# Optimization experiments

Measured on AMD Instinct MI355X. Metric: run time of the kernel, lower is better.

## Reference

```python
import jax, jax.numpy as jnp
import numpy as np


def conv2d(x, w, b=None, pad=0):
    # x: [B,C,H,W], w: [O,I,kh,kw]
    out = jax.lax.conv_general_dilated(
        x, w, window_strides=(1, 1), padding=[(pad, pad), (pad, pad)],
        dimension_numbers=('NCHW', 'OIHW', 'NCHW'))
    if b is not None:
        out = out + b[None, :, None, None]
    return out


def setup_inputs() -> dict:
    key = jax.random.key(0)
    ks = jax.random.split(key, 10)
    B, C, W, H, N, G = 8, 256, 64, 64, 1024, 32
    s = jnp.float32(0.02)  # small init so softmax is not saturated
    return {
        'input_graph': jax.random.normal(ks[0], (B, N, G), jnp.float32),
        'input_image': jax.random.normal(ks[1], (B, C, W, H), jnp.float32),
        'Wq': jax.random.normal(ks[2], (C, C), jnp.float32) * s,
        'bq': jnp.zeros((C,), jnp.float32),
        'Wk': jax.random.normal(ks[3], (C, G), jnp.float32) * s,
        'bk': jnp.zeros((C,), jnp.float32),
        'Wv': jax.random.normal(ks[4], (C, G), jnp.float32) * s,
        'bv': jnp.zeros((C,), jnp.float32),
        'conv1_w': jax.random.normal(ks[5], (C, C, 1, 1), jnp.float32) * s,
        'bn_gamma': jnp.ones((C,), jnp.float32),
        'bn_beta': jnp.zeros((C,), jnp.float32),
        'bn_mean': jnp.zeros((C,), jnp.float32),
        'bn_var': jnp.ones((C,), jnp.float32),
        'conv2_w': jax.random.normal(ks[6], (C, C, 3, 3), jnp.float32) * s,
        'conv2_b': jnp.zeros((C,), jnp.float32),
        'conv3_w': jax.random.normal(ks[7], (C, C, 1, 1), jnp.float32) * s,
        'conv3_b': jnp.zeros((C,), jnp.float32),
    }


def reference(input_graph, input_image, Wq, bq, Wk, bk, Wv, bv,
              conv1_w, bn_gamma, bn_beta, bn_mean, bn_var,
              conv2_w, conv2_b, conv3_w, conv3_b):
    B, C, W, H = input_image.shape
    P = W * H
    g = jnp.transpose(input_graph, (0, 2, 1))  # [B,G,N]
    # 1x1 conv1d projections == per-position matmuls
    K = jnp.einsum('og,bgn->bon', Wk, g) + bk[None, :, None]   # [B,C,N]
    V = jnp.einsum('og,bgn->bon', Wv, g) + bv[None, :, None]   # [B,C,N]
    x = input_image.reshape(B, C, P)
    Q = jnp.einsum('oc,bcp->bop', Wq, x) + bq[None, :, None]   # [B,C,P]
    # att[b,p,n] = sum_c Q[b,c,p] * K[b,c,n]  (Q was permuted to [B,P,C] in torch)
    att = jnp.einsum('bcp,bcn->bpn', Q, K) / jnp.sqrt(jnp.float32(C))
    # NOTE: original applies Softmax(dim=1) -> over the P (pixel) axis
    att = jax.nn.softmax(att, axis=1)
    # message = V @ att^T : [B,C,N] x [B,N,P] -> [B,C,P]
    msg = jnp.einsum('bcn,bpn->bcp', V, att).reshape(B, C, W, H)
    # Conv_Bn_Activation: 1x1 conv (no bias) + BN (inference) + LeakyReLU(0.1)
    h = conv2d(msg, conv1_w)
    inv = jax.lax.rsqrt(bn_var + jnp.float32(1e-5))
    h = (h - bn_mean[None, :, None, None]) * (bn_gamma * inv)[None, :, None, None] + bn_beta[None, :, None, None]
    h = jnp.where(h > 0, h, jnp.float32(0.1) * h)
    h = conv2d(h, conv2_w, conv2_b, pad=1)  # 3x3, pad 1
    return input_image + conv2d(h, conv3_w, conv3_b)  # 1x1
```

## Files before the change

### kernel.cpp

```cpp
#include <hip/hip_runtime.h>
#include <hip/hip_bf16.h>

typedef __hip_bfloat16 bf16;
typedef unsigned short u16;
typedef __attribute__((ext_vector_type(8))) short  b8v;
typedef __attribute__((ext_vector_type(8))) unsigned short u16x8;
typedef __attribute__((ext_vector_type(4))) unsigned short u16x4;
typedef __attribute__((ext_vector_type(4))) float f32x4;

static __device__ __forceinline__ float us2f(u16 s) {
    unsigned int u = ((unsigned int)s) << 16;
    return __builtin_bit_cast(float, u);
}
static __device__ __forceinline__ u16 f2us(float x) {
    union { bf16 h; u16 s; } v; v.h = __float2bfloat16(x); return v.s;
}
static __device__ __forceinline__ float b2f(bf16 x) { return __bfloat162float(x); }
static __device__ __forceinline__ bf16 f2b(float x) { return __float2bfloat16(x); }
static __device__ __forceinline__ float toF(float x) { return x; }
static __device__ __forceinline__ float toF(bf16 x)  { return b2f(x); }
static __device__ __forceinline__ void stor(float* p, float v) { *p = v; }
static __device__ __forceinline__ void stor(bf16* p,  float v) { *p = f2b(v); }

static __device__ __forceinline__ void gload16(const u16* g, u16* l) {
    __builtin_amdgcn_global_load_lds(
        (const __attribute__((address_space(1))) unsigned int*)g,
        (__attribute__((address_space(3))) unsigned int*)l,
        16, 0, 0);
}


__global__ __launch_bounds__(256) void cast_f2b4(const float* __restrict__ src,
                                                 u16* __restrict__ dst, int n4)
{
    int i = blockIdx.x * 256 + threadIdx.x;
    if (i < n4) {
        float4 v = ((const float4*)src)[i];
        u16x4 o = { f2us(v.x), f2us(v.y), f2us(v.z), f2us(v.w) };
        ((u16x4*)dst)[i] = o;
    }
}

__global__ __launch_bounds__(256) void repack_w2(const float* __restrict__ src,
                                                 u16* __restrict__ dst)
{
    int idx = blockIdx.x * 256 + threadIdx.x;
    int o = idx / 2304, k = idx - o * 2304;
    int tap = k >> 8, c = k & 255;
    dst[idx] = f2us(src[(o * 256 + c) * 9 + tap]);
}

__global__ __launch_bounds__(256) void transpose_cast_x(const float* __restrict__ x,
                                                        u16* __restrict__ xT, int C, int P)
{
    __shared__ u16 t[64][72];
    const int b = blockIdx.z, c0 = blockIdx.y * 64, p0 = blockIdx.x * 64;
    const int tid = threadIdx.x;
    const int r = tid >> 2, q = tid & 3;
    const float* src = x + ((size_t)b * C + c0 + r) * P + p0 + q * 16;
#pragma unroll
    for (int i = 0; i < 16; i++) t[q * 16 + i][r] = f2us(src[i]);
    __syncthreads();
    u16* dst = xT + ((size_t)b * P + p0 + r) * C + c0 + q * 16;
    *(u16x8*)dst       = *(u16x8*)&t[r][q * 16];
    *(u16x8*)(dst + 8) = *(u16x8*)&t[r][q * 16 + 8];
}

template<int EPI, typename TA, typename TB, typename TC>
__global__ __launch_bounds__(256) void gemm_any(
    const TA* __restrict__ A, const TB* __restrict__ B, TC* __restrict__ C,
    int M, int Nn, int Kd,
    long saM, long saK, long aB,
    long sbK, long sbN, long bB,
    long scM, long scN, long cB,
    float scale, const float* __restrict__ bias)
{
    __shared__ float As[16][65];
    __shared__ float Bs[16][65];
    const int b  = blockIdx.z;
    const TA* Ab = A + (long)b * aB;
    const TB* Bb = B + (long)b * bB;
    const int m0 = blockIdx.y * 64, n0 = blockIdx.x * 64;
    const int tid = threadIdx.x;
    const int tx = tid & 15, ty = tid >> 4;
    const bool kfA = (saK == 1);
    const bool nfB = (sbN == 1);
    float acc[4][4] = {};

    for (int k0 = 0; k0 < Kd; k0 += 16) {
#pragma unroll
        for (int i = 0; i < 4; i++) {
            int idx = tid + i * 256; int mm, kk;
            if (kfA) { kk = idx & 15; mm = idx >> 4; }
            else     { mm = idx & 63; kk = idx >> 6; }
            As[kk][mm] = toF(Ab[(long)(m0 + mm) * saM + (long)(k0 + kk) * saK]);
        }
#pragma unroll
        for (int i = 0; i < 4; i++) {
            int idx = tid + i * 256; int nn, kk;
            if (nfB) { nn = idx & 63; kk = idx >> 6; }
            else     { kk = idx & 15; nn = idx >> 4; }
            Bs[kk][nn] = toF(Bb[(long)(k0 + kk) * sbK + (long)(n0 + nn) * sbN]);
        }
        __syncthreads();
#pragma unroll
        for (int kk = 0; kk < 16; kk++) {
            float a[4], bb[4];
#pragma unroll
            for (int i = 0; i < 4; i++) a[i]  = As[kk][ty * 4 + i];
#pragma unroll
            for (int j = 0; j < 4; j++) bb[j] = Bs[kk][tx * 4 + j];
#pragma unroll
            for (int i = 0; i < 4; i++)
#pragma unroll
                for (int j = 0; j < 4; j++) acc[i][j] += a[i] * bb[j];
        }
        __syncthreads();
    }
#pragma unroll
    for (int i = 0; i < 4; i++) {
        int m = m0 + ty * 4 + i;
        float add0 = (EPI == 0 && bias) ? bias[m] : 0.f;
#pragma unroll
        for (int j = 0; j < 4; j++) {
            int n = n0 + tx * 4 + j;
            float v = acc[i][j] * scale + add0;
            if (EPI == 3 && bias) v += bias[n];
            stor(&C[(long)b * cB + (long)m * scM + (long)n * scN], v);
        }
    }
}

template<int EPI, bool CT, typename TC, int NTILE>
__global__ __launch_bounds__(256) void gemm_mfma(
    const u16* __restrict__ A, const u16* __restrict__ Bt, TC* __restrict__ Cc,
    int M, int N, int K, int lda, int ldb, int ldc,
    long aBat, long bBat, long cBat,
    float scale, const float* __restrict__ bias,
    const float* __restrict__ gamma, const float* __restrict__ beta,
    const float* __restrict__ mean,  const float* __restrict__ var,
    const float* __restrict__ resid, long rBat, int ldr,
    float* __restrict__ csum)
{
    constexpr int NI = NTILE / 32;
    __shared__ u16 Al[128 * 32];
    __shared__ u16 Bl[NTILE * 32];
    __shared__ float red[(EPI == 3) ? 256 : 1];
    __shared__ u16 tbuf[(EPI == 3) ? 64 * 136 : 1];
    const int bat = blockIdx.z;
    const int m0 = blockIdx.y * 128, n0 = blockIdx.x * NTILE;
    const int tid = threadIdx.x;
    const int lane = tid & 63, wid = tid >> 6;
    const int wr = wid >> 1, wc = wid & 1;
    const int fr = lane & 15, fq = lane >> 4;
    const int sc = ((lane & 3) ^ ((lane >> 3) & 3)) * 8;
    const int axs = (fq ^ ((fr >> 1) & 3)) * 8;

    const u16* gA = A  + (size_t)bat * aBat + (size_t)(m0 + wid * 32 + (lane >> 2)) * lda + sc;
    const u16* gB = Bt + (size_t)bat * bBat + (size_t)(n0 + wid * (NTILE / 4) + (lane >> 2)) * ldb + sc;
    u16* lA = &Al[(wid * 32) * 32];
    u16* lB = &Bl[(wid * (NTILE / 4)) * 32];
    const size_t a16 = (size_t)16 * lda, b16 = (size_t)16 * ldb;

    f32x4 acc[4][NI];
#pragma unroll
    for (int i = 0; i < 4; i++)
#pragma unroll
        for (int j = 0; j < NI; j++) acc[i][j] = (f32x4){0.f, 0.f, 0.f, 0.f};

    for (int k0 = 0; k0 < K; k0 += 32) {
        gload16(gA + k0,       lA);
        gload16(gA + k0 + a16, lA + 16 * 32);
        gload16(gB + k0,       lB);
        if constexpr (NTILE == 128) gload16(gB + k0 + b16, lB + 16 * 32);
        __syncthreads();
        b8v a[4], b[NI];
#pragma unroll
        for (int mi = 0; mi < 4; mi++) a[mi] = *(const b8v*)&Al[(wr * 64 + mi * 16 + fr) * 32 + axs];
#pragma unroll
        for (int ni = 0; ni < NI; ni++) b[ni] = *(const b8v*)&Bl[(wc * (NTILE / 2) + ni * 16 + fr) * 32 + axs];
#pragma unroll
        for (int mi = 0; mi < 4; mi++)
#pragma unroll
            for (int ni = 0; ni < NI; ni++)
                acc[mi][ni] = __builtin_amdgcn_mfma_f32_16x16x32_bf16(a[mi], b[ni], acc[mi][ni], 0, 0, 0);
        __syncthreads();
    }

    const int mbase = m0 + wr * 64, nbase = n0 + wc * (NTILE / 2);

    if constexpr (EPI == 3) {
        float cs[NI];
#pragma unroll
        for (int ni = 0; ni < NI; ni++) cs[ni] = 0.f;
#pragma unroll
        for (int h = 0; h < 2; h++) {
#pragma unroll
            for (int mh = 0; mh < 2; mh++) {
                const int mi = h * 2 + mh;
                const int trow = wr * 32 + mh * 16 + fq * 4;
#pragma unroll
                for (int ni = 0; ni < NI; ni++) {
                    const int n = nbase + ni * 16 + fr;
                    const float tqv = bias ? bias[(size_t)bat * N + n] : 0.f;
                    f32x4 v = acc[mi][ni];
#pragma unroll
                    for (int j = 0; j < 4; j++) {
                        float x = __expf((v[j] + tqv) * scale);
                        cs[ni] += x;
                        tbuf[(trow + j) * 136 + wc * 64 + ni * 16 + fr] = f2us(x);
                    }
                }
            }
            __syncthreads();
#pragma unroll
            for (int it = 0; it < 4; it++) {
                const int idx = it * 256 + tid;
                const int row = idx >> 4, ng = idx & 15;
                const int m = m0 + (row >> 5) * 64 + h * 32 + (row & 31);
                u16x8 v8 = *(const u16x8*)&tbuf[row * 136 + ng * 8];
                *(u16x8*)((u16*)Cc + (size_t)bat * cBat + (size_t)m * ldc + n0 + ng * 8) = v8;
            }
            __syncthreads();
        }
#pragma unroll
        for (int ni = 0; ni < NI; ni++) {
            float s = cs[ni];
            s += __shfl_xor(s, 16, 64);
            s += __shfl_xor(s, 32, 64);
            if (fq == 0) red[wr * 128 + wc * 64 + ni * 16 + fr] = s;
        }
        __syncthreads();
        if (tid < NTILE) {
            float s = red[tid] + red[128 + tid];
            csum[((size_t)bat * gridDim.y + blockIdx.y) * ldc + n0 + tid] = s;
        }
        return;
    }

#pragma unroll
    for (int mi = 0; mi < 4; mi++) {
        float esc[4], ead[4];
#pragma unroll
        for (int j = 0; j < 4; j++) {
            int m = mbase + mi * 16 + fq * 4 + j;
            if (EPI == 1) {
                float sc2 = gamma[m] * rsqrtf(var[m] + 1e-5f);
                esc[j] = sc2; ead[j] = beta[m] - mean[m] * sc2;
            } else {
                esc[j] = scale;
                ead[j] = ((EPI == 0 || EPI == 2) && bias) ? bias[m] : 0.f;
            }
        }
#pragma unroll
        for (int ni = 0; ni < NI; ni++) {
            f32x4 v = acc[mi][ni];
            const int n = nbase + ni * 16 + fr;
            if (CT) {
                const int mb = mbase + mi * 16 + fq * 4;
                if constexpr (EPI == 4) {
                    const float bb = bias ? bias[n] : 0.f;
                    float4 rv = *(const float4*)&resid[(size_t)bat * rBat + (size_t)n * ldr + mb];
                    float4 o4;
                    o4.x = v[0] * scale + bb + rv.x;
                    o4.y = v[1] * scale + bb + rv.y;
                    o4.z = v[2] * scale + bb + rv.z;
                    o4.w = v[3] * scale + bb + rv.w;
                    *(float4*)((float*)Cc + (size_t)bat * cBat + (size_t)n * ldc + mb) = o4;
                } else {
                    const long crow = (EPI == 1)
                        ? (long)(((n >> 6) + 1) * 66 + (n & 63) + 1)
                        : (long)n;
                    u16x4 pk;
#pragma unroll
                    for (int j = 0; j < 4; j++) {
                        float x = v[j] * esc[j] + ead[j];
                        if (EPI == 1) x = x > 0.f ? x : 0.1f * x;
                        pk[j] = f2us(x);
                    }
                    *(u16x4*)((u16*)Cc + (size_t)bat * cBat + (size_t)crow * ldc + mb) = pk;
                }
            } else {
#pragma unroll
                for (int j = 0; j < 4; j++) {
                    int m = mbase + mi * 16 + fq * 4 + j;
                    float x = v[j] * esc[j] + ead[j];
                    if (EPI == 1) x = x > 0.f ? x : 0.1f * x;
                    if (EPI == 2) x += resid[(size_t)bat * rBat + (size_t)m * ldr + n];
                    TC* p = Cc + (size_t)bat * cBat + (size_t)m * ldc + n;
                    if constexpr (sizeof(TC) == 2) *(u16*)p = f2us(x); else *(float*)p = x;
                }
            }
        }
    }
}

__global__ __launch_bounds__(256) void conv3x3_mfma(
    const u16* __restrict__ Wt, const u16* __restrict__ Xp, u16* __restrict__ Y,
    const float* __restrict__ bias)
{
    const int C = 256, P = 4096, K = 2304;
    __shared__ u16 Al[2][128 * 32];
    __shared__ u16 Bl[64 * 64];
    const int bat = blockIdx.z;
    const int m0 = blockIdx.y * 128;
    const int y0 = blockIdx.x;
    const int tid = threadIdx.x;
    const int lane = tid & 63, wid = tid >> 6;
    const int wr = wid >> 1, wc = wid & 1;
    const int fr = lane & 15, fq = lane >> 4;
    const int scA = ((lane & 3) ^ ((lane >> 3) & 3)) * 8;
    const int axs = (fq ^ ((fr >> 1) & 3)) * 8;

    const u16* Ag = Wt + (size_t)(m0 + wid * 32 + (lane >> 2)) * K + scA;
    u16* lA0 = &Al[0][(wid * 32) * 32];
    u16* lA1 = &Al[1][(wid * 32) * 32];
    const u16* Xb = Xp + (size_t)bat * 66 * 66 * 256;

    const int brow = (lane >> 3), bq = lane & 7;

    f32x4 acc[4][2];
#pragma unroll
    for (int i = 0; i < 4; i++)
#pragma unroll
        for (int j = 0; j < 2; j++) acc[i][j] = (f32x4){0.f, 0.f, 0.f, 0.f};

    for (int k0 = 0; k0 < K; k0 += 64) {
        const int tap = k0 >> 8, c0k = k0 & 255;
        const int dy = tap / 3 - 1, dxv = tap - (tap / 3) * 3 - 1;
        const int syp = y0 + dy + 1;
        gload16(Ag + k0,                       lA0);
        gload16(Ag + k0 + (size_t)16 * K,      lA0 + 16 * 32);
        gload16(Ag + k0 + 32,                  lA1);
        gload16(Ag + k0 + 32 + (size_t)16 * K, lA1 + 16 * 32);
#pragma unroll
        for (int h = 0; h < 2; h++) {
            const int g = wid * 2 + h;
            const int r = g * 8 + brow;
            const int qs = bq ^ (r & 7);
            const u16* src = Xb + ((size_t)syp * 66 + (r + dxv + 1)) * 256 + c0k + qs * 8;
            gload16(src, &Bl[g * 512]);
        }
        __syncthreads();
#pragma unroll
        for (int t = 0; t < 2; t++) {
            b8v a[4], b[2];
#pragma unroll
            for (int mi = 0; mi < 4; mi++) a[mi] = *(const b8v*)&Al[t][(wr * 64 + mi * 16 + fr) * 32 + axs];
#pragma unroll
            for (int ni = 0; ni < 2; ni++) {
                const int row = wc * 32 + ni * 16 + fr;
                const int ch = ((t * 4 + fq) ^ (fr & 7)) * 8;
                b[ni] = *(const b8v*)&Bl[row * 64 + ch];
            }
#pragma unroll
            for (int mi = 0; mi < 4; mi++)
#pragma unroll
                for (int ni = 0; ni < 2; ni++)
                    acc[mi][ni] = __builtin_amdgcn_mfma_f32_16x16x32_bf16(a[mi], b[ni], acc[mi][ni], 0, 0, 0);
        }
        __syncthreads();
    }

    const int mbase = m0 + wr * 64, nbase = y0 * 64 + wc * 32;
#pragma unroll
    for (int mi = 0; mi < 4; mi++) {
        const int mb = mbase + mi * 16 + fq * 4;
        float bb[4];
#pragma unroll
        for (int j = 0; j < 4; j++) bb[j] = bias[mb + j];
#pragma unroll
        for (int ni = 0; ni < 2; ni++) {
            const int n = nbase + ni * 16 + fr;
            u16x4 pk;
#pragma unroll
            for (int j = 0; j < 4; j++) pk[j] = f2us(acc[mi][ni][j] + bb[j]);
            *(u16x4*)&Y[(size_t)bat * P * C + (size_t)n * C + mb] = pk;
        }
    }
}


__global__ __launch_bounds__(256) void tq_dot(const u16* __restrict__ Kt,
                                              const float* __restrict__ bq,
                                              float* __restrict__ tq, int N, int C)
{
    const int n = blockIdx.x * 256 + threadIdx.x, b = blockIdx.y;
    const u16* row = Kt + ((size_t)b * N + n) * C;
    float s = 0.f;
    for (int c = 0; c < C; c += 8) {
        u16x8 v = *(const u16x8*)&row[c];
#pragma unroll
        for (int j = 0; j < 8; j++) s += us2f(v[j]) * bq[c + j];
    }
    tq[(size_t)b * N + n] = s;
}

__global__ __launch_bounds__(256) void colsum_merge(const float* __restrict__ part,
                                                    float* __restrict__ sinv, int N, int PC)
{
    const int n = blockIdx.x * 256 + threadIdx.x, b = blockIdx.y;
    const float* pc = part + (size_t)b * PC * N + n;
    float s = 0.f;
    for (int c = 0; c < PC; c++) s += pc[(size_t)c * N];
    sinv[(size_t)b * N + n] = 1.f / s;
}

__global__ __launch_bounds__(256) void scale_vt(u16* __restrict__ Vt,
                                                const float* __restrict__ sinv,
                                                int N, int C)
{
    const size_t base = ((size_t)blockIdx.x * 256 + threadIdx.x) * 8;
    const int n = (int)((base / C) % N);
    const int b = (int)(base / ((size_t)N * C));
    const float s = sinv[(size_t)b * N + n];
    u16x8 v = *(u16x8*)&Vt[base];
#pragma unroll
    for (int j = 0; j < 8; j++) v[j] = f2us(us2f(v[j]) * s);
    *(u16x8*)&Vt[base] = v;
}

__global__ __launch_bounds__(256) void zero_halo(u16* __restrict__ Xp)
{
    int i = blockIdx.x * 256 + threadIdx.x;
    const int ch8 = i & 31; i >>= 5;
    const int hp = i % 260;
    const int b = i / 260;
    int py, px;
    if (hp < 66)       { py = 0;  px = hp; }
    else if (hp < 132) { py = 65; px = hp - 66; }
    else if (hp < 196) { py = hp - 132 + 1; px = 0; }
    else               { py = hp - 196 + 1; px = 65; }
    u16x8 z = {0, 0, 0, 0, 0, 0, 0, 0};
    *(u16x8*)&Xp[(((size_t)b * 66 + py) * 66 + px) * 256 + ch8 * 8] = z;
}


extern "C" void kernel_launch(void* const* d_in, const int* in_sizes, int n_in,
                              void* d_out, int out_size, void* d_ws, size_t ws_size,
                              hipStream_t stream)
{
    const float* graph = (const float*)d_in[0];
    const float* image = (const float*)d_in[1];
    const float* Wq  = (const float*)d_in[2];
    const float* bq  = (const float*)d_in[3];
    const float* Wk  = (const float*)d_in[4];
    const float* bk  = (const float*)d_in[5];
    const float* Wv  = (const float*)d_in[6];
    const float* bv  = (const float*)d_in[7];
    const float* c1w = (const float*)d_in[8];
    const float* gam = (const float*)d_in[9];
    const float* bet = (const float*)d_in[10];
    const float* mea = (const float*)d_in[11];
    const float* var = (const float*)d_in[12];
    const float* c2w = (const float*)d_in[13];
    const float* c2b = (const float*)d_in[14];
    const float* c3w = (const float*)d_in[15];
    const float* c3b = (const float*)d_in[16];
    float* out = (float*)d_out;

    const int B = 8, C = 256, P = 4096, N = 1024, G = 32;
    const size_t MiB = 1024 * 1024, KiB = 1024;
    char* ws = (char*)d_ws;
    char* dob = (char*)d_out;
    u16* WqT  = (u16*)(ws);
    u16* E    = (u16*)(ws);
    u16* xT   = (u16*)(ws + 64 * MiB);
    u16* Kt   = (u16*)(ws + 80 * MiB);
    u16* VV   = (u16*)(ws + 80 * MiB);
    u16* Vt   = (u16*)(ws + 84 * MiB);
    u16* h2T  = (u16*)(ws);
    u16* c2w_b = (u16*)(ws + 17 * MiB);
    u16* c3w_b = (u16*)(ws + 19 * MiB);
    float* part = (float*)(dob);
    u16* KWt   = (u16*)(dob + 2 * MiB);
    float* tqb = (float*)(dob + 6 * MiB);
    float* sinv = (float*)(dob + 7 * MiB);
    u16* c1w_b = (u16*)(dob + 8 * MiB);
    u16* h1p   = (u16*)(dob + 14 * MiB);

    transpose_cast_x<<<dim3(P / 64, C / 64, B), 256, 0, stream>>>(image, xT, C, P);
    transpose_cast_x<<<dim3(4, 4, 1), 256, 0, stream>>>(Wq, WqT, 256, 256);
    cast_f2b4<<<64, 256, 0, stream>>>(c1w, c1w_b, 16384);
    gemm_any<3, float, float, bf16><<<dim3(C / 64, N / 64, B), 256, 0, stream>>>(
        graph, Wk, (bf16*)Kt, N, C, G,
        G, 1, (long)N * G,   1, G, 0,   C, 1, (long)N * C, 1.f, bk);
    gemm_any<3, float, float, bf16><<<dim3(C / 64, N / 64, B), 256, 0, stream>>>(
        graph, Wv, (bf16*)Vt, N, C, G,
        G, 1, (long)N * G,   1, G, 0,   C, 1, (long)N * C, 1.f, bv);
    gemm_mfma<0, false, u16, 64><<<dim3(C / 64, N / 128, B), 256, 0, stream>>>(
        Kt, WqT, KWt, N, C, C, C, C, C,
        (long)N * C, 0, (long)N * C, 1.f, nullptr,
        nullptr, nullptr, nullptr, nullptr, nullptr, 0, 0, nullptr);
    tq_dot<<<dim3(N / 256, B), 256, 0, stream>>>(Kt, bq, tqb, N, C);
    gemm_mfma<3, false, u16, 128><<<dim3(N / 128, P / 128, B), 256, 0, stream>>>(
        xT, KWt, E, P, N, C, C, C, N,
        (long)P * C, (long)N * C, (long)P * N, 0.0625f, tqb,
        nullptr, nullptr, nullptr, nullptr, nullptr, 0, 0, part);
    colsum_merge<<<dim3(N / 256, B), 256, 0, stream>>>(part, sinv, N, P / 128);
    scale_vt<<<dim3((int)((size_t)B * N * C / 8 / 256)), 256, 0, stream>>>(Vt, sinv, N, C);
    gemm_mfma<0, false, u16, 64><<<dim3(N / 64, C / 128, B), 256, 0, stream>>>(
        c1w_b, Vt, VV, C, N, C, C, C, N,
        0, (long)N * C, (long)C * N, 1.f, nullptr,
        nullptr, nullptr, nullptr, nullptr, nullptr, 0, 0, nullptr);
    gemm_mfma<1, true, u16, 64><<<dim3(P / 64, C / 128, B), 256, 0, stream>>>(
        VV, E, h1p, C, P, N, N, N, C,
        (long)C * N, (long)P * N, (long)66 * 66 * C, 1.f, nullptr,
        gam, bet, mea, var, nullptr, 0, 0, nullptr);
    zero_halo<<<260, 256, 0, stream>>>(h1p);
    repack_w2<<<2304, 256, 0, stream>>>(c2w, c2w_b);
    cast_f2b4<<<64, 256, 0, stream>>>(c3w, c3w_b, 16384);
    conv3x3_mfma<<<dim3(P / 64, C / 128, B), 256, 0, stream>>>(c2w_b, h1p, h2T, c2b);
    gemm_mfma<4, true, float, 64><<<dim3(C / 64, P / 128, B), 256, 0, stream>>>(
        h2T, c3w_b, out, P, C, C, C, C, P,
        (long)P * C, 0, (long)C * P, 1.f, c3b,
        nullptr, nullptr, nullptr, nullptr, image, (long)C * P, P, nullptr);
}
```

Before: 229.9 us.

## Fold K/Q and V/conv1 weights algebraically, swizzle MFMA block order, widen tiles

Precomputes Wk^T·Wq and conv1·Wv (plus bias folds) so the K·Wq and conv1·V products become small G=32 GEMMs straight from the graph input. This removes the K/V projection GEMMs, the two 256-deep MFMA GEMMs, tq_dot and scale_vt, and folds the softmax column normaliser into the VV epilogue. It also adds a block-index swizzle to gemm_mfma for L2 locality, widens the N tile of the message GEMM to 128, changes an LDS swizzle index in the conv, and moves zero_halo earlier. The folds change rounding order, and the conv swizzle edit risks correctness if it does not match the write side.

```diff
diff --git a/kernel.cpp b/kernel.cpp
--- a/kernel.cpp
+++ b/kernel.cpp
@@ -64,6 +64,72 @@
     u16* dst = xT + ((size_t)b * P + p0 + r) * C + c0 + q * 16;
     *(u16x8*)dst       = *(u16x8*)&t[r][q * 16];
     *(u16x8*)(dst + 8) = *(u16x8*)&t[r][q * 16 + 8];
+}
+
+__global__ __launch_bounds__(256) void fold_k(const float* __restrict__ Wk,
+                                              const float* __restrict__ Wq,
+                                              const float* __restrict__ bk,
+                                              const float* __restrict__ bq,
+                                              float* __restrict__ WkWq, float* __restrict__ kqb,
+                                              float* __restrict__ wkbq, float* __restrict__ bqbk)
+{
+    const int g = blockIdx.x;
+    const int c = threadIdx.x;
+    float s = 0.f;
+#pragma unroll 8
+    for (int o = 0; o < 256; o++) s += Wk[o * 32 + g] * Wq[o * 256 + c];
+    WkWq[g * 256 + c] = s;
+    if (blockIdx.x == 0) {
+        float t = 0.f;
+#pragma unroll 8
+        for (int o = 0; o < 256; o++) t += bk[o] * Wq[o * 256 + c];
+        kqb[c] = t;
+    }
+    if (threadIdx.x == 0) {
+        float u = 0.f;
+#pragma unroll 8
+        for (int o = 0; o < 256; o++) u += bq[o] * Wk[o * 32 + g];
+        wkbq[g] = u;
+    }
+    if (blockIdx.x == 0 && threadIdx.x == 1) {
+        float u = 0.f;
+#pragma unroll 8
+        for (int o = 0; o < 256; o++) u += bq[o] * bk[o];
+        bqbk[0] = u;
+    }
+}
+
+__global__ __launch_bounds__(64) void fold_v(const float* __restrict__ c1w,
+                                             const float* __restrict__ Wv,
+                                             const float* __restrict__ bv,
+                                             float* __restrict__ W1V, float* __restrict__ b1v)
+{
+    const int o = blockIdx.x;
+    const int g = threadIdx.x;
+    if (g < 32) {
+        float s = 0.f;
+#pragma unroll 8
+        for (int c = 0; c < 256; c++) s += c1w[o * 256 + c] * Wv[c * 32 + g];
+        W1V[o * 32 + g] = s;
+    } else if (g == 32) {
+        float s = 0.f;
+#pragma unroll 8
+        for (int c = 0; c < 256; c++) s += c1w[o * 256 + c] * bv[c];
+        b1v[o] = s;
+    }
+}
+
+__global__ __launch_bounds__(256) void tq_small(const float* __restrict__ graph,
+                                                const float* __restrict__ wkbq,
+                                                const float* __restrict__ bqbk,
+                                                float* __restrict__ tq, int N, int G)
+{
+    const int n = blockIdx.x * 256 + threadIdx.x, b = blockIdx.y;
+    const float* row = graph + ((size_t)b * N + n) * G;
+    float s = bqbk[0];
+#pragma unroll
+    for (int g = 0; g < 32; g++) s += row[g] * wkbq[g];
+    tq[(size_t)b * N + n] = s;
 }
 
 template<int EPI, typename TA, typename TB, typename TC>
@@ -73,7 +139,7 @@
     long saM, long saK, long aB,
     long sbK, long sbN, long bB,
     long scM, long scN, long cB,
-    float scale, const float* __restrict__ bias)
+    float scale, const float* __restrict__ bias, const float* __restrict__ scl)
 {
     __shared__ float As[16][65];
     __shared__ float Bs[16][65];
@@ -120,12 +186,13 @@
 #pragma unroll
     for (int i = 0; i < 4; i++) {
         int m = m0 + ty * 4 + i;
-        float add0 = (EPI == 0 && bias) ? bias[m] : 0.f;
+        float add0 = ((EPI == 0 || EPI == 4) && bias) ? bias[m] : 0.f;
 #pragma unroll
         for (int j = 0; j < 4; j++) {
             int n = n0 + tx * 4 + j;
             float v = acc[i][j] * scale + add0;
             if (EPI == 3 && bias) v += bias[n];
+            if (EPI == 4) v *= scl[(long)b * Nn + n];
             stor(&C[(long)b * cB + (long)m * scM + (long)n * scN], v);
         }
     }
@@ -148,7 +215,11 @@
     __shared__ float red[(EPI == 3) ? 256 : 1];
     __shared__ u16 tbuf[(EPI == 3) ? 64 * 136 : 1];
     const int bat = blockIdx.z;
-    const int m0 = blockIdx.y * 128, n0 = blockIdx.x * NTILE;
+    const int nxy = gridDim.x * gridDim.y;
+    const int fid = blockIdx.y * gridDim.x + blockIdx.x;
+    const int swzid = (fid & 7) * (nxy >> 3) + (fid >> 3);
+    const int bidx = swzid % gridDim.x, bidy = swzid / gridDim.x;
+    const int m0 = bidy * 128, n0 = bidx * NTILE;
     const int tid = threadIdx.x;
     const int lane = tid & 63, wid = tid >> 6;
     const int wr = wid >> 1, wc = wid & 1;
@@ -233,7 +304,7 @@
         __syncthreads();
         if (tid < NTILE) {
             float s = red[tid] + red[128 + tid];
-            csum[((size_t)bat * gridDim.y + blockIdx.y) * ldc + n0 + tid] = s;
+            csum[((size_t)bat * gridDim.y + bidy) * ldc + n0 + tid] = s;
         }
         return;
     }
@@ -249,7 +320,7 @@
                 esc[j] = sc2; ead[j] = beta[m] - mean[m] * sc2;
             } else {
                 esc[j] = scale;
-                ead[j] = ((EPI == 0 || EPI == 2) && bias) ? bias[m] : 0.f;
+                ead[j] = 0.f;
             }
         }
 #pragma unroll
@@ -286,7 +357,6 @@
                     int m = mbase + mi * 16 + fq * 4 + j;
                     float x = v[j] * esc[j] + ead[j];
                     if (EPI == 1) x = x > 0.f ? x : 0.1f * x;
-                    if (EPI == 2) x += resid[(size_t)bat * rBat + (size_t)m * ldr + n];
                     TC* p = Cc + (size_t)bat * cBat + (size_t)m * ldc + n;
                     if constexpr (sizeof(TC) == 2) *(u16*)p = f2us(x); else *(float*)p = x;
                 }
@@ -350,7 +420,7 @@
 #pragma unroll
             for (int ni = 0; ni < 2; ni++) {
                 const int row = wc * 32 + ni * 16 + fr;
-                const int ch = ((t * 4 + fq) ^ (fr & 7)) * 8;
+                const int ch = ((t * 4 + fq) ^ (row & 7)) * 8;
                 b[ni] = *(const b8v*)&Bl[row * 64 + ch];
             }
 #pragma unroll
@@ -380,21 +450,6 @@
     }
 }
 
-
-__global__ __launch_bounds__(256) void tq_dot(const u16* __restrict__ Kt,
-                                              const float* __restrict__ bq,
-                                              float* __restrict__ tq, int N, int C)
-{
-    const int n = blockIdx.x * 256 + threadIdx.x, b = blockIdx.y;
-    const u16* row = Kt + ((size_t)b * N + n) * C;
-    float s = 0.f;
-    for (int c = 0; c < C; c += 8) {
-        u16x8 v = *(const u16x8*)&row[c];
-#pragma unroll
-        for (int j = 0; j < 8; j++) s += us2f(v[j]) * bq[c + j];
-    }
-    tq[(size_t)b * N + n] = s;
-}
 
 __global__ __launch_bounds__(256) void colsum_merge(const float* __restrict__ part,
                                                     float* __restrict__ sinv, int N, int PC)
@@ -404,20 +459,6 @@
     float s = 0.f;
     for (int c = 0; c < PC; c++) s += pc[(size_t)c * N];
     sinv[(size_t)b * N + n] = 1.f / s;
-}
-
-__global__ __launch_bounds__(256) void scale_vt(u16* __restrict__ Vt,
-                                                const float* __restrict__ sinv,
-                                                int N, int C)
-{
-    const size_t base = ((size_t)blockIdx.x * 256 + threadIdx.x) * 8;
-    const int n = (int)((base / C) % N);
-    const int b = (int)(base / ((size_t)N * C));
-    const float s = sinv[(size_t)b * N + n];
-    u16x8 v = *(u16x8*)&Vt[base];
-#pragma unroll
-    for (int j = 0; j < 8; j++) v[j] = f2us(us2f(v[j]) * s);
-    *(u16x8*)&Vt[base] = v;
 }
 
 __global__ __launch_bounds__(256) void zero_halo(u16* __restrict__ Xp)
@@ -463,12 +504,9 @@
     const size_t MiB = 1024 * 1024, KiB = 1024;
     char* ws = (char*)d_ws;
     char* dob = (char*)d_out;
-    u16* WqT  = (u16*)(ws);
     u16* E    = (u16*)(ws);
     u16* xT   = (u16*)(ws + 64 * MiB);
-    u16* Kt   = (u16*)(ws + 80 * MiB);
     u16* VV   = (u16*)(ws + 80 * MiB);
-    u16* Vt   = (u16*)(ws + 84 * MiB);
     u16* h2T  = (u16*)(ws);
     u16* c2w_b = (u16*)(ws + 17 * MiB);
     u16* c3w_b = (u16*)(ws + 19 * MiB);
@@ -476,38 +514,34 @@
     u16* KWt   = (u16*)(dob + 2 * MiB);
     float* tqb = (float*)(dob + 6 * MiB);
     float* sinv = (float*)(dob + 7 * MiB);
-    u16* c1w_b = (u16*)(dob + 8 * MiB);
+    float* WkWq = (float*)(dob + 8 * MiB);
+    float* kqb  = (float*)(dob + 8 * MiB + 64 * KiB);
+    float* wkbq = (float*)(dob + 8 * MiB + 128 * KiB);
+    float* bqbk = (float*)(dob + 8 * MiB + 160 * KiB);
+    float* W1V  = (float*)(dob + 9 * MiB);
+    float* b1v  = (float*)(dob + 9 * MiB + 64 * KiB);
     u16* h1p   = (u16*)(dob + 14 * MiB);
 
     transpose_cast_x<<<dim3(P / 64, C / 64, B), 256, 0, stream>>>(image, xT, C, P);
-    transpose_cast_x<<<dim3(4, 4, 1), 256, 0, stream>>>(Wq, WqT, 256, 256);
-    cast_f2b4<<<64, 256, 0, stream>>>(c1w, c1w_b, 16384);
+    fold_k<<<32, 256, 0, stream>>>(Wk, Wq, bk, bq, WkWq, kqb, wkbq, bqbk);
+    fold_v<<<256, 64, 0, stream>>>(c1w, Wv, bv, W1V, b1v);
+    zero_halo<<<260, 256, 0, stream>>>(h1p);
     gemm_any<3, float, float, bf16><<<dim3(C / 64, N / 64, B), 256, 0, stream>>>(
-        graph, Wk, (bf16*)Kt, N, C, G,
-        G, 1, (long)N * G,   1, G, 0,   C, 1, (long)N * C, 1.f, bk);
-    gemm_any<3, float, float, bf16><<<dim3(C / 64, N / 64, B), 256, 0, stream>>>(
-        graph, Wv, (bf16*)Vt, N, C, G,
-        G, 1, (long)N * G,   1, G, 0,   C, 1, (long)N * C, 1.f, bv);
-    gemm_mfma<0, false, u16, 64><<<dim3(C / 64, N / 128, B), 256, 0, stream>>>(
-        Kt, WqT, KWt, N, C, C, C, C, C,
-        (long)N * C, 0, (long)N * C, 1.f, nullptr,
-        nullptr, nullptr, nullptr, nullptr, nullptr, 0, 0, nullptr);
-    tq_dot<<<dim3(N / 256, B), 256, 0, stream>>>(Kt, bq, tqb, N, C);
+        graph, WkWq, (bf16*)KWt, N, C, G,
+        G, 1, (long)N * G,   C, 1, 0,   C, 1, (long)N * C, 1.f, kqb, nullptr);
+    tq_small<<<dim3(N / 256, B), 256, 0, stream>>>(graph, wkbq, bqbk, tqb, N, G);
     gemm_mfma<3, false, u16, 128><<<dim3(N / 128, P / 128, B), 256, 0, stream>>>(
         xT, KWt, E, P, N, C, C, C, N,
         (long)P * C, (long)N * C, (long)P * N, 0.0625f, tqb,
         nullptr, nullptr, nullptr, nullptr, nullptr, 0, 0, part);
     colsum_merge<<<dim3(N / 256, B), 256, 0, stream>>>(part, sinv, N, P / 128);
-    scale_vt<<<dim3((int)((size_t)B * N * C / 8 / 256)), 256, 0, stream>>>(Vt, sinv, N, C);
-    gemm_mfma<0, false, u16, 64><<<dim3(N / 64, C / 128, B), 256, 0, stream>>>(
-        c1w_b, Vt, VV, C, N, C, C, C, N,
-        0, (long)N * C, (long)C * N, 1.f, nullptr,
-        nullptr, nullptr, nullptr, nullptr, nullptr, 0, 0, nullptr);
-    gemm_mfma<1, true, u16, 64><<<dim3(P / 64, C / 128, B), 256, 0, stream>>>(
+    gemm_any<4, float, float, bf16><<<dim3(N / 64, C / 64, B), 256, 0, stream>>>(
+        W1V, graph, (bf16*)VV, C, N, G,
+        G, 1, 0,   1, G, (long)N * G,   N, 1, (long)C * N, 1.f, b1v, sinv);
+    gemm_mfma<1, true, u16, 128><<<dim3(P / 128, C / 128, B), 256, 0, stream>>>(
         VV, E, h1p, C, P, N, N, N, C,
         (long)C * N, (long)P * N, (long)66 * 66 * C, 1.f, nullptr,
         gam, bet, mea, var, nullptr, 0, 0, nullptr);
-    zero_halo<<<260, 256, 0, stream>>>(h1p);
     repack_w2<<<2304, 256, 0, stream>>>(c2w, c2w_b);
     cast_f2b4<<<64, 256, 0, stream>>>(c3w, c3w_b, 16384);
     conv3x3_mfma<<<dim3(P / 64, C / 128, B), 256, 0, stream>>>(c2w_b, h1p, h2T, c2b);
```

Measured after the change: 235.0 us. +2.2%, slower.
